# Kernel optimization log

Hardware: AMD Instinct MI355X
Metric: run time of the kernel (lower is better)

The kernel has to match this reference:

```python
import jax, jax.numpy as jnp
import numpy as np

BLOCK_SIZE = 16
E2M1_LOOKUP = jnp.array([0.0, 0.5, 1.0, 1.5, 2.0, 3.0, 4.0, 6.0], dtype=jnp.float32)


def setup_inputs() -> dict:
    key = jax.random.key(0)
    k1, k2, k3, k4, k5 = jax.random.split(key, 5)
    in_features, out_features = 8192, 8192
    x = jax.random.normal(k1, (64, in_features), dtype=jnp.float32)
    weight_packed = jax.random.randint(k2, (out_features, in_features // 2), 0, 256, dtype=jnp.int32)
    weight_scale = jax.random.uniform(k3, (out_features, in_features // BLOCK_SIZE), dtype=jnp.float32)
    weight_global_scale = jax.random.uniform(k4, (1,), dtype=jnp.float32) + 0.5
    bias = jax.random.normal(k5, (out_features,), dtype=jnp.float32)
    return {"x": x, "weight_packed": weight_packed, "weight_scale": weight_scale,
            "weight_global_scale": weight_global_scale, "bias": bias}


def unpack_nvfp4(weight_packed, weight_scale, weight_global_scale, dtype=jnp.float32):
    out_features, in_packed = weight_packed.shape
    in_features = in_packed * 2
    low = weight_packed & 15
    high = (weight_packed >> 4) & 15
    # per-byte order: low nibble first, then high nibble
    combined = jnp.stack([low, high], axis=-1).reshape(out_features, in_features)
    signs = (combined >> 3) & 1
    mag_idx = combined & 7
    values = E2M1_LOOKUP[mag_idx] * (1.0 - 2.0 * signs.astype(jnp.float32))
    # per-block (16-wide) scale
    values = (values.reshape(out_features, -1, BLOCK_SIZE) * weight_scale[..., None]).reshape(out_features, in_features)
    g = weight_global_scale.reshape(())
    actual_scale = jnp.where(g != 0, 1.0 / g, 1.0)
    return (values * actual_scale).astype(dtype)


def reference(x, weight_packed, weight_scale, weight_global_scale, bias):
    W = unpack_nvfp4(weight_packed, weight_scale, weight_global_scale, dtype=x.dtype)
    return x @ W.T + bias
```

## Files before the change

### kernel.cpp

```cpp
#include <hip/hip_runtime.h>
#include <stdint.h>

typedef _Float16 f16x2 __attribute__((ext_vector_type(2)));
typedef _Float16 f16x8 __attribute__((ext_vector_type(8)));
typedef float f32x4 __attribute__((ext_vector_type(4)));

static __device__ __forceinline__ uint32_t perm(uint32_t hi, uint32_t lo, uint32_t sel) {
    return __builtin_amdgcn_perm(hi, lo, sel);
}
static __device__ __forceinline__ f16x2 bch2(uint32_t u) { union { uint32_t x; f16x2 h; } c; c.x = u; return c.h; }
static __device__ __forceinline__ uint32_t bcu(f16x2 h) { union { uint32_t x; f16x2 h; } c; c.h = h; return c.x; }
static __device__ __forceinline__ uint32_t pkrtz(float a, float b) {
    auto r = __builtin_amdgcn_cvt_pkrtz(a, b);
    union { decltype(r) h; uint32_t u; } c; c.h = r; return c.u;
}

#define NTOT 8192
#define KTOT 8192
#define SPLITS 8
#define KCHUNK 1024
#define BN 256
#define QK 256

__global__ __launch_bounds__(256, 2) void nvfp4_init_out(const float* __restrict__ bias,
                                                         float* __restrict__ out) {
    int i = blockIdx.x * 256 + threadIdx.x;
    ((f32x4*)out)[i] = ((const f32x4*)bias)[i & 2047];
}

__global__ __launch_bounds__(256, 2) void nvfp4_reduce(const float* __restrict__ part,
                                                       const float* __restrict__ bias,
                                                       float* __restrict__ out) {
    int i = blockIdx.x * 256 + threadIdx.x;
    f32x4 s = ((const f32x4*)bias)[i & 2047];
    #pragma unroll
    for (int p = 0; p < SPLITS; ++p) {
        f32x4 v = ((const f32x4*)part)[(size_t)p * 131072 + i];
        s = s + v;
    }
    ((f32x4*)out)[i] = s;
}

__global__ __launch_bounds__(512, 2) void nvfp4_gemm(const float* __restrict__ x,
                                                     const int* __restrict__ wp,
                                                     const float* __restrict__ wscale,
                                                     const float* __restrict__ gs,
                                                     float* __restrict__ dst,
                                                     int atomic_mode) {
    __shared__ __align__(16) uint8_t xl[2][64 * 256 * 2];
    __shared__ uint32_t sl[256 * 65];

    const int tid = threadIdx.x;
    const int nb = blockIdx.x & 31;
    const int ksp = blockIdx.x >> 5;
    const int nbase = nb * BN;
    const int kc0 = ksp * KCHUNK;

    {
        float g = gs[0];
        float inv_g = (g != 0.0f) ? (1.0f / g) : 1.0f;
        int row = tid >> 1;
        int cb = (tid & 1) * 32;
        const f32x4* sp = (const f32x4*)(wscale + (size_t)(nbase + row) * 512 + ksp * 64 + cb);
        uint32_t* d = sl + row * 65 + cb;
        #pragma unroll
        for (int q = 0; q < 8; ++q) {
            f32x4 v = sp[q];
            float a0 = v.x * inv_g, a1 = v.y * inv_g, a2 = v.z * inv_g, a3 = v.w * inv_g;
            d[q * 4 + 0] = pkrtz(a0, a0);
            d[q * 4 + 1] = pkrtz(a1, a1);
            d[q * 4 + 2] = pkrtz(a2, a2);
            d[q * 4 + 3] = pkrtz(a3, a3);
        }
    }

    const int lane = tid & 63;
    const int wid = tid >> 6;
    const int l15 = lane & 15;
    const int grp = lane >> 4;

    const int sa = tid >> 5;
    const int scb = (tid & 31) * 8;
    const float* xbase = x + (size_t)sa * KTOT + kc0 + scb;

    auto xload = [&](int q, f32x4* r) {
        const float* p = xbase + q * QK;
        #pragma unroll
        for (int j = 0; j < 4; ++j) {
            r[j * 2 + 0] = *(const f32x4*)(p + (size_t)j * 16 * KTOT);
            r[j * 2 + 1] = *(const f32x4*)(p + (size_t)j * 16 * KTOT + 4);
        }
    };
    auto xwrite = [&](int b, const f32x4* r) {
        #pragma unroll
        for (int j = 0; j < 4; ++j) {
            int row = sa + j * 16;
            uint4 d;
            d.x = pkrtz(r[j * 2].x, r[j * 2].y);
            d.y = pkrtz(r[j * 2].z, r[j * 2].w);
            d.z = pkrtz(r[j * 2 + 1].x, r[j * 2 + 1].y);
            d.w = pkrtz(r[j * 2 + 1].z, r[j * 2 + 1].w);
            uint32_t addr = ((uint32_t)(row * 512 + scb * 2)) ^ ((row & 7) << 4);
            *(uint4*)(xl[b] + addr) = d;
        }
    };

    f32x4 acc[4][2];
    #pragma unroll
    for (int a = 0; a < 4; ++a)
        #pragma unroll
        for (int b = 0; b < 2; ++b)
            acc[a][b] = f32x4{0.f, 0.f, 0.f, 0.f};

    const uint32_t TH = 0x46444240u, TL = 0x3E3C3800u;

    const int wrow0 = nbase + wid * 32 + l15;
    const int* wq0 = wp + (size_t)wrow0 * 4096 + (kc0 >> 1) + grp * 4;
    const int* wq1 = wp + (size_t)(wrow0 + 16) * 4096 + (kc0 >> 1) + grp * 4;
    const int srow0 = (wid * 32 + l15) * 65;
    const int srow1 = (wid * 32 + 16 + l15) * 65;

    f32x4 sA[8], sB[8];
    xload(0, sA);
    int4 w0[3], w1[3];
    w0[0] = *(const int4*)(wq0);
    w1[0] = *(const int4*)(wq1);
    w0[1] = *(const int4*)(wq0 + 16);
    w1[1] = *(const int4*)(wq1 + 16);
    xwrite(0, sA);
    xload(1, sB);
    __syncthreads();

    #pragma unroll
    for (int t = 0; t < 32; ++t) {
        const int rb = (t >> 3) & 1;
        const int tq = t & 7;
        if (t < 30) {
            w0[(t + 2) % 3] = *(const int4*)(wq0 + (t + 2) * 16);
            w1[(t + 2) % 3] = *(const int4*)(wq1 + (t + 2) * 16);
        }
        f16x8 af[4];
        #pragma unroll
        for (int mt = 0; mt < 4; ++mt) {
            int row = mt * 16 + l15;
            uint32_t addr = ((uint32_t)(row * 512 + (tq * 32 + grp * 8) * 2)) ^ ((row & 7) << 4);
            af[mt] = *(const f16x8*)(xl[rb] + addr);
        }
        const int scol = t * 2 + (grp >> 1);
        f16x2 s2a = bch2(sl[srow0 + scol]);
        f16x2 s2b = bch2(sl[srow1 + scol]);

        #pragma unroll
        for (int ss = 0; ss < 2; ++ss) {
            const int4 w4 = ss ? w1[t % 3] : w0[t % 3];
            const f16x2 s2 = ss ? s2b : s2a;
            uint32_t b = (uint32_t)(w4.x & 0xff) | ((uint32_t)(w4.y & 0xff) << 8) |
                         ((uint32_t)(w4.z & 0xff) << 16) | ((uint32_t)w4.w << 24);
            uint32_t sel_e = b & 0x07070707u;
            uint32_t sel_o = (b >> 4) & 0x07070707u;
            uint32_t he = perm(TH, TL, sel_e) | ((b & 0x08080808u) << 4);
            uint32_t ho = perm(TH, TL, sel_o) | (b & 0x80808080u);
            uint32_t d0 = perm(ho, he, 0x040C000Cu);
            uint32_t d1 = perm(ho, he, 0x050C010Cu);
            uint32_t d2 = perm(ho, he, 0x060C020Cu);
            uint32_t d3 = perm(ho, he, 0x070C030Cu);
            union { uint32_t u[4]; f16x8 h; } fr;
            fr.u[0] = bcu(bch2(d0) * s2);
            fr.u[1] = bcu(bch2(d1) * s2);
            fr.u[2] = bcu(bch2(d2) * s2);
            fr.u[3] = bcu(bch2(d3) * s2);
            #pragma unroll
            for (int mt = 0; mt < 4; ++mt)
                acc[mt][ss] = __builtin_amdgcn_mfma_f32_16x16x32_f16(af[mt], fr.h, acc[mt][ss], 0, 0, 0);
        }

        if ((t & 7) == 7 && t < 31) {
            const int q = t >> 3;
            if (q == 0) { xwrite(1, sB); xload(2, sA); }
            if (q == 1) { xwrite(0, sA); xload(3, sB); }
            if (q == 2) { xwrite(1, sB); }
            __syncthreads();
        }
    }

    if (atomic_mode) {
        #pragma unroll
        for (int mt = 0; mt < 4; ++mt)
            #pragma unroll
            for (int ss = 0; ss < 2; ++ss)
                #pragma unroll
                for (int q = 0; q < 4; ++q) {
                    int row = mt * 16 + grp * 4 + q;
                    int col = nbase + wid * 32 + ss * 16 + l15;
                    unsafeAtomicAdd(dst + (size_t)row * NTOT + col, acc[mt][ss][q]);
                }
    } else {
        float* pd = dst + (size_t)ksp * 64 * NTOT;
        #pragma unroll
        for (int mt = 0; mt < 4; ++mt)
            #pragma unroll
            for (int ss = 0; ss < 2; ++ss)
                #pragma unroll
                for (int q = 0; q < 4; ++q) {
                    int row = mt * 16 + grp * 4 + q;
                    int col = nbase + wid * 32 + ss * 16 + l15;
                    pd[(size_t)row * NTOT + col] = acc[mt][ss][q];
                }
    }
}

extern "C" void kernel_launch(void* const* d_in, const int* in_sizes, int n_in,
                              void* d_out, int out_size, void* d_ws, size_t ws_size,
                              hipStream_t stream) {
    const float* x = (const float*)d_in[0];
    const int* wp = (const int*)d_in[1];
    const float* wscale = (const float*)d_in[2];
    const float* gs = (const float*)d_in[3];
    const float* bias = (const float*)d_in[4];
    float* out = (float*)d_out;

    const size_t need = (size_t)SPLITS * 64 * NTOT * sizeof(float);
    if (ws_size >= need) {
        nvfp4_gemm<<<dim3(SPLITS * (NTOT / BN)), dim3(512), 0, stream>>>(x, wp, wscale, gs, (float*)d_ws, 0);
        nvfp4_reduce<<<dim3(512), dim3(256), 0, stream>>>((const float*)d_ws, bias, out);
    } else {
        nvfp4_init_out<<<dim3(512), dim3(256), 0, stream>>>(bias, out);
        nvfp4_gemm<<<dim3(SPLITS * (NTOT / BN)), dim3(512), 0, stream>>>(x, wp, wscale, gs, out, 1);
    }
}
```

Baseline: 221.4 us.

## Stage packed weights through LDS with coalesced loads and double-buffered 128-K phases

Packed weights were loaded directly per lane into registers with a 3-deep prefetch. They are now loaded cooperatively with coalesced 16-byte loads, compressed to one byte per int, and written to a swizzled, double-buffered LDS tile. The x staging is also reworked into 128-K phases with a new XOR swizzle, and scales are stored as 16-bit halves. This trades direct register prefetch for better global coalescing, at the cost of extra LDS traffic and a barrier per phase with a rolled loop.

```diff
diff --git a/kernel.cpp b/kernel.cpp
--- a/kernel.cpp
+++ b/kernel.cpp
@@ -20,7 +20,8 @@
 #define SPLITS 8
 #define KCHUNK 1024
 #define BN 256
-#define QK 256
+#define PK 128
+#define NPER (KCHUNK / PK)
 
 __global__ __launch_bounds__(256, 2) void nvfp4_init_out(const float* __restrict__ bias,
                                                          float* __restrict__ out) {
@@ -47,8 +48,9 @@
                                                      const float* __restrict__ gs,
                                                      float* __restrict__ dst,
                                                      int atomic_mode) {
-    __shared__ __align__(16) uint8_t xl[2][64 * 256 * 2];
-    __shared__ uint32_t sl[256 * 65];
+    __shared__ uint32_t wl[2][256 * 16];
+    __shared__ __align__(16) uint8_t xtl[2][64 * 256];
+    __shared__ uint16_t scl[256 * 66];
 
     const int tid = threadIdx.x;
     const int nb = blockIdx.x & 31;
@@ -56,54 +58,75 @@
     const int nbase = nb * BN;
     const int kc0 = ksp * KCHUNK;
 
+    const int lane = tid & 63;
+    const int wid = tid >> 6;
+    const int l15 = lane & 15;
+    const int grp = lane >> 4;
+
+    const int wsrow = tid >> 4;
+    const int wss = tid & 15;
+    const int* wgp = wp + (size_t)(nbase + wsrow) * 4096 + (kc0 >> 1) + wss * 4;
+    const int xsrow = tid >> 3;
+    const int xss = tid & 7;
+    const float* xgp = x + (size_t)xsrow * KTOT + kc0 + xss * 4;
+
+    int4 wst[8];
+    f32x4 xst[4];
+
+    auto issueW = [&](int p) {
+        #pragma unroll
+        for (int i = 0; i < 8; ++i)
+            wst[i] = *(const int4*)(wgp + (size_t)i * 32 * 4096 + p * 64);
+    };
+    auto issueX = [&](int p) {
+        #pragma unroll
+        for (int j = 0; j < 4; ++j)
+            xst[j] = *(const f32x4*)(xgp + p * 128 + j * 32);
+    };
+    auto writeW = [&](int p) {
+        uint32_t* wb = wl[p & 1];
+        #pragma unroll
+        for (int i = 0; i < 8; ++i) {
+            int R = wsrow + i * 32;
+            uint32_t v = (uint32_t)(wst[i].x & 0xff) | ((uint32_t)(wst[i].y & 0xff) << 8) |
+                         ((uint32_t)(wst[i].z & 0xff) << 16) | ((uint32_t)wst[i].w << 24);
+            wb[R * 16 + (wss ^ (R & 15))] = v;
+        }
+    };
+    auto writeX = [&](int p) {
+        uint8_t* xb = xtl[p & 1];
+        #pragma unroll
+        for (int j = 0; j < 4; ++j) {
+            uint32_t lo = pkrtz(xst[j].x, xst[j].y);
+            uint32_t hi = pkrtz(xst[j].z, xst[j].w);
+            int slot = j * 4 + (xss >> 1);
+            uint32_t addr = (uint32_t)(xsrow * 256 + ((slot ^ (xsrow & 15)) << 4) + (xss & 1) * 8);
+            uint2 dv; dv.x = lo; dv.y = hi;
+            *(uint2*)(xb + addr) = dv;
+        }
+    };
+
+    issueW(0);
+    issueX(0);
     {
         float g = gs[0];
         float inv_g = (g != 0.0f) ? (1.0f / g) : 1.0f;
         int row = tid >> 1;
-        int cb = (tid & 1) * 32;
-        const f32x4* sp = (const f32x4*)(wscale + (size_t)(nbase + row) * 512 + ksp * 64 + cb);
-        uint32_t* d = sl + row * 65 + cb;
-        #pragma unroll
-        for (int q = 0; q < 8; ++q) {
-            f32x4 v = sp[q];
-            float a0 = v.x * inv_g, a1 = v.y * inv_g, a2 = v.z * inv_g, a3 = v.w * inv_g;
-            d[q * 4 + 0] = pkrtz(a0, a0);
-            d[q * 4 + 1] = pkrtz(a1, a1);
-            d[q * 4 + 2] = pkrtz(a2, a2);
-            d[q * 4 + 3] = pkrtz(a3, a3);
-        }
-    }
-
-    const int lane = tid & 63;
-    const int wid = tid >> 6;
-    const int l15 = lane & 15;
-    const int grp = lane >> 4;
-
-    const int sa = tid >> 5;
-    const int scb = (tid & 31) * 8;
-    const float* xbase = x + (size_t)sa * KTOT + kc0 + scb;
-
-    auto xload = [&](int q, f32x4* r) {
-        const float* p = xbase + q * QK;
-        #pragma unroll
-        for (int j = 0; j < 4; ++j) {
-            r[j * 2 + 0] = *(const f32x4*)(p + (size_t)j * 16 * KTOT);
-            r[j * 2 + 1] = *(const f32x4*)(p + (size_t)j * 16 * KTOT + 4);
-        }
-    };
-    auto xwrite = [&](int b, const f32x4* r) {
-        #pragma unroll
-        for (int j = 0; j < 4; ++j) {
-            int row = sa + j * 16;
-            uint4 d;
-            d.x = pkrtz(r[j * 2].x, r[j * 2].y);
-            d.y = pkrtz(r[j * 2].z, r[j * 2].w);
-            d.z = pkrtz(r[j * 2 + 1].x, r[j * 2 + 1].y);
-            d.w = pkrtz(r[j * 2 + 1].z, r[j * 2 + 1].w);
-            uint32_t addr = ((uint32_t)(row * 512 + scb * 2)) ^ ((row & 7) << 4);
-            *(uint4*)(xl[b] + addr) = d;
-        }
-    };
+        int half = tid & 1;
+        const float* sp = wscale + (size_t)(nbase + row) * 512 + (kc0 >> 4) + half * 32;
+        #pragma unroll
+        for (int j = 0; j < 8; ++j) {
+            f32x4 v = *(const f32x4*)(sp + j * 4);
+            uint32_t p01 = pkrtz(v.x * inv_g, v.y * inv_g);
+            uint32_t p23 = pkrtz(v.z * inv_g, v.w * inv_g);
+            uint32_t c = half * 32 + j * 4;
+            *(uint32_t*)((uint8_t*)scl + row * 132 + c * 2) = p01;
+            *(uint32_t*)((uint8_t*)scl + row * 132 + c * 2 + 4) = p23;
+        }
+    }
+    writeW(0);
+    writeX(0);
+    __syncthreads();
 
     f32x4 acc[4][2];
     #pragma unroll
@@ -113,74 +136,57 @@
             acc[a][b] = f32x4{0.f, 0.f, 0.f, 0.f};
 
     const uint32_t TH = 0x46444240u, TL = 0x3E3C3800u;
-
-    const int wrow0 = nbase + wid * 32 + l15;
-    const int* wq0 = wp + (size_t)wrow0 * 4096 + (kc0 >> 1) + grp * 4;
-    const int* wq1 = wp + (size_t)(wrow0 + 16) * 4096 + (kc0 >> 1) + grp * 4;
-    const int srow0 = (wid * 32 + l15) * 65;
-    const int srow1 = (wid * 32 + 16 + l15) * 65;
-
-    f32x4 sA[8], sB[8];
-    xload(0, sA);
-    int4 w0[3], w1[3];
-    w0[0] = *(const int4*)(wq0);
-    w1[0] = *(const int4*)(wq1);
-    w0[1] = *(const int4*)(wq0 + 16);
-    w1[1] = *(const int4*)(wq1 + 16);
-    xwrite(0, sA);
-    xload(1, sB);
-    __syncthreads();
-
-    #pragma unroll
-    for (int t = 0; t < 32; ++t) {
-        const int rb = (t >> 3) & 1;
-        const int tq = t & 7;
-        if (t < 30) {
-            w0[(t + 2) % 3] = *(const int4*)(wq0 + (t + 2) * 16);
-            w1[(t + 2) % 3] = *(const int4*)(wq1 + (t + 2) * 16);
-        }
-        f16x8 af[4];
-        #pragma unroll
-        for (int mt = 0; mt < 4; ++mt) {
-            int row = mt * 16 + l15;
-            uint32_t addr = ((uint32_t)(row * 512 + (tq * 32 + grp * 8) * 2)) ^ ((row & 7) << 4);
-            af[mt] = *(const f16x8*)(xl[rb] + addr);
-        }
-        const int scol = t * 2 + (grp >> 1);
-        f16x2 s2a = bch2(sl[srow0 + scol]);
-        f16x2 s2b = bch2(sl[srow1 + scol]);
-
-        #pragma unroll
-        for (int ss = 0; ss < 2; ++ss) {
-            const int4 w4 = ss ? w1[t % 3] : w0[t % 3];
-            const f16x2 s2 = ss ? s2b : s2a;
-            uint32_t b = (uint32_t)(w4.x & 0xff) | ((uint32_t)(w4.y & 0xff) << 8) |
-                         ((uint32_t)(w4.z & 0xff) << 16) | ((uint32_t)w4.w << 24);
-            uint32_t sel_e = b & 0x07070707u;
-            uint32_t sel_o = (b >> 4) & 0x07070707u;
-            uint32_t he = perm(TH, TL, sel_e) | ((b & 0x08080808u) << 4);
-            uint32_t ho = perm(TH, TL, sel_o) | (b & 0x80808080u);
-            uint32_t d0 = perm(ho, he, 0x040C000Cu);
-            uint32_t d1 = perm(ho, he, 0x050C010Cu);
-            uint32_t d2 = perm(ho, he, 0x060C020Cu);
-            uint32_t d3 = perm(ho, he, 0x070C030Cu);
-            union { uint32_t u[4]; f16x8 h; } fr;
-            fr.u[0] = bcu(bch2(d0) * s2);
-            fr.u[1] = bcu(bch2(d1) * s2);
-            fr.u[2] = bcu(bch2(d2) * s2);
-            fr.u[3] = bcu(bch2(d3) * s2);
-            #pragma unroll
-            for (int mt = 0; mt < 4; ++mt)
-                acc[mt][ss] = __builtin_amdgcn_mfma_f32_16x16x32_f16(af[mt], fr.h, acc[mt][ss], 0, 0, 0);
-        }
-
-        if ((t & 7) == 7 && t < 31) {
-            const int q = t >> 3;
-            if (q == 0) { xwrite(1, sB); xload(2, sA); }
-            if (q == 1) { xwrite(0, sA); xload(3, sB); }
-            if (q == 2) { xwrite(1, sB); }
-            __syncthreads();
-        }
+    const int srowb0 = (wid * 32 + l15) * 132;
+    const int srowb1 = (wid * 32 + 16 + l15) * 132;
+    const int wR0 = wid * 32 + l15;
+    const int wR1 = wid * 32 + 16 + l15;
+
+    for (int p = 0; p < NPER; ++p) {
+        if (p + 1 < NPER) { issueW(p + 1); issueX(p + 1); }
+        const uint32_t* wb = wl[p & 1];
+        const uint8_t* xb = xtl[p & 1];
+
+        #pragma unroll
+        for (int tl = 0; tl < 4; ++tl) {
+            f16x8 af[4];
+            #pragma unroll
+            for (int mt = 0; mt < 4; ++mt) {
+                int row = mt * 16 + l15;
+                uint32_t addr = (uint32_t)(row * 256 + (((tl * 4 + grp) ^ l15) << 4));
+                af[mt] = *(const f16x8*)(xb + addr);
+            }
+            int scol = p * 8 + tl * 2 + (grp >> 1);
+            uint32_t sr0 = *(const uint16_t*)((const uint8_t*)scl + srowb0 + scol * 2);
+            uint32_t sr1 = *(const uint16_t*)((const uint8_t*)scl + srowb1 + scol * 2);
+            f16x2 s2a = bch2(perm(0, sr0, 0x01000100u));
+            f16x2 s2b = bch2(perm(0, sr1, 0x01000100u));
+
+            #pragma unroll
+            for (int ss = 0; ss < 2; ++ss) {
+                const int R = ss ? wR1 : wR0;
+                const f16x2 s2 = ss ? s2b : s2a;
+                uint32_t b = wb[R * 16 + ((tl * 4 + grp) ^ l15)];
+                uint32_t sel_e = b & 0x07070707u;
+                uint32_t sel_o = (b >> 4) & 0x07070707u;
+                uint32_t he = perm(TH, TL, sel_e) | ((b & 0x08080808u) << 4);
+                uint32_t ho = perm(TH, TL, sel_o) | (b & 0x80808080u);
+                uint32_t d0 = perm(ho, he, 0x040C000Cu);
+                uint32_t d1 = perm(ho, he, 0x050C010Cu);
+                uint32_t d2 = perm(ho, he, 0x060C020Cu);
+                uint32_t d3 = perm(ho, he, 0x070C030Cu);
+                union { uint32_t u[4]; f16x8 h; } fr;
+                fr.u[0] = bcu(bch2(d0) * s2);
+                fr.u[1] = bcu(bch2(d1) * s2);
+                fr.u[2] = bcu(bch2(d2) * s2);
+                fr.u[3] = bcu(bch2(d3) * s2);
+                #pragma unroll
+                for (int mt = 0; mt < 4; ++mt)
+                    acc[mt][ss] = __builtin_amdgcn_mfma_f32_16x16x32_f16(af[mt], fr.h, acc[mt][ss], 0, 0, 0);
+            }
+        }
+
+        if (p + 1 < NPER) { writeW(p + 1); writeX(p + 1); }
+        __syncthreads();
     }
 
     if (atomic_mode) {
```

Result: no change. 220.2 us (-0.5%).
